# Optimization experiments

Measured on AMD Instinct MI355X. Metric: run time of the kernel, lower is better.

Reference implementation:

```python
import jax, jax.numpy as jnp
import numpy as np


def setup_inputs() -> dict:
    key = jax.random.key(0)
    ks = jax.random.split(key, 5)
    B, C, H, W = 4, 64, 64, 64
    C8 = C // 8
    return {
        "x_opt": jax.random.normal(ks[0], (B, C, H, W), jnp.float32),
        "x_sar": jax.random.normal(ks[1], (B, C, H, W), jnp.float32),
        "wq": jax.random.normal(ks[2], (C8, C), jnp.float32) * 0.05,
        "bq": jnp.zeros((C8,), jnp.float32),
        "wk": jax.random.normal(ks[3], (C8, C), jnp.float32) * 0.05,
        "bk": jnp.zeros((C8,), jnp.float32),
        "wv": jax.random.normal(ks[4], (C, C), jnp.float32) * 0.05,
        "bv": jnp.zeros((C,), jnp.float32),
        "gamma": jnp.zeros((1,), jnp.float32),
    }


def reference(x_opt, x_sar, wq, bq, wk, bk, wv, bv, gamma):
    b, c, h, w = x_opt.shape
    n = h * w
    xo = x_opt.reshape(b, c, n)  # [b, c, N]
    xs = x_sar.reshape(b, c, n)
    # 1x1 convs == channel matmuls
    q = jnp.einsum('oc,bcn->bon', wq, xo) + bq[None, :, None]  # [b, c//8, N]
    k = jnp.einsum('oc,bcn->bon', wk, xs) + bk[None, :, None]  # [b, c//8, N]
    v = jnp.einsum('oc,bcn->bon', wv, xs) + bv[None, :, None]  # [b, c, N]
    # attn[b, n, m] = softmax_m( q[:, :, n] . k[:, :, m] )  -- NO 1/sqrt(d) scaling
    scores = jnp.einsum('bdn,bdm->bnm', q, k)  # [b, N, N]
    attn = jax.nn.softmax(scores, axis=-1)
    # out[b, c, n] = sum_m v[b, c, m] * attn[b, n, m]
    out = jnp.einsum('bcm,bnm->bcn', v, attn).reshape(b, c, h, w)
    return gamma[0] * out + x_opt
```

## Files before the change

kernel.cpp:

```cpp
#include <hip/hip_runtime.h>
#include <hip/hip_bf16.h>
#include <stdint.h>

#define NDIM 4096
#define CDIM 64
#define NSPLIT 8
#define SPAN (NDIM / NSPLIT)
#define NQ4 (SPAN / 32)
#define LOG2E 1.44269504088896f

typedef float f32x4 __attribute__((ext_vector_type(4)));
typedef float f32x16 __attribute__((ext_vector_type(16)));
typedef short bf16x8 __attribute__((ext_vector_type(8)));
union U4B { uint4 u; bf16x8 b; };

static __device__ __forceinline__ uint32_t cvtpk(float lo, float hi) {
  uint32_t r;
  asm("v_cvt_pk_bf16_f32 %0, %1, %2" : "=v"(r) : "v"(lo), "v"(hi));
  return r;
}
static __device__ __forceinline__ uint16_t f2bf(float f) {
  uint32_t r;
  asm("v_cvt_pk_bf16_f32 %0, %1, %1" : "=v"(r) : "v"(f));
  return (uint16_t)r;
}
static __device__ __forceinline__ float fexp2(float x) {
  return __builtin_amdgcn_exp2f(x);
}

__global__ __launch_bounds__(256) void proj_kernel(
    const float* __restrict__ x_opt, const float* __restrict__ x_sar,
    const float* __restrict__ wq, const float* __restrict__ bq,
    const float* __restrict__ wk, const float* __restrict__ bk,
    const float* __restrict__ wvp, const float* __restrict__ bv,
    uint16_t* __restrict__ qf, uint16_t* __restrict__ kfp,
    uint16_t* __restrict__ vf2)
{
  const int tid = threadIdx.x;
  const int w = tid >> 6;
  const int l = tid & 63;
  const int x = l & 31;
  const int hi = l >> 5;

  const int id = blockIdx.x;
  const int b = id >> 7;
  const int n0 = (id & 127) * 32;
  const size_t xbase = (size_t)b * CDIM * NDIM;

  const float* xsrc = (w == 2) ? x_opt : x_sar;
  bf16x8 xB[4];
#pragma unroll
  for (int kc = 0; kc < 4; kc++) {
    float sv[8];
#pragma unroll
    for (int j = 0; j < 8; j++)
      sv[j] = xsrc[xbase + (size_t)(kc * 16 + hi * 8 + j) * NDIM + n0 + x];
    U4B us;
    us.u = make_uint4(cvtpk(sv[0], sv[1]), cvtpk(sv[2], sv[3]),
                      cvtpk(sv[4], sv[5]), cvtpk(sv[6], sv[7]));
    xB[kc] = us.b;
  }

  bf16x8 aF[4];
#pragma unroll
  for (int kc = 0; kc < 4; kc++) {
    U4B ua;
    ua.u = make_uint4(0u, 0u, 0u, 0u);
    if (w < 2) {
      const float* wr = wvp + (w * 32 + x) * 64 + kc * 16 + hi * 8;
      float4 wa = ((const float4*)wr)[0];
      float4 wb = ((const float4*)wr)[1];
      ua.u = make_uint4(cvtpk(wa.x, wa.y), cvtpk(wa.z, wa.w),
                        cvtpk(wb.x, wb.y), cvtpk(wb.z, wb.w));
    } else if (x < 8) {
      const float* wr = ((w == 2) ? wq : wk) + x * 64 + kc * 16 + hi * 8;
      float4 wa = ((const float4*)wr)[0];
      float4 wb = ((const float4*)wr)[1];
      ua.u = make_uint4(cvtpk(wa.x, wa.y), cvtpk(wa.z, wa.w),
                        cvtpk(wb.x, wb.y), cvtpk(wb.z, wb.w));
    }
    aF[kc] = ua.b;
  }

  const f32x16 z16 = {0.f,0.f,0.f,0.f, 0.f,0.f,0.f,0.f,
                      0.f,0.f,0.f,0.f, 0.f,0.f,0.f,0.f};
  f32x16 acc = z16;
#pragma unroll
  for (int kc = 0; kc < 4; kc++)
    acc = __builtin_amdgcn_mfma_f32_32x32x16_bf16(aF[kc], xB[kc], acc, 0, 0, 0);

  if (w < 2) {
    const size_t kbbase = (size_t)b * 256 + (n0 >> 4) + (x >> 4);
    const int kk = x & 15;
#pragma unroll
    for (int r = 0; r < 16; r++) {
      const int row = w * 32 + (r & 3) + 8 * (r >> 2) + 4 * hi;
      vf2[(kbbase * 64 + row) * 16 + kk] = f2bf(acc[r] + bv[row]);
    }
  } else if (w == 2) {
    float gv[4];
#pragma unroll
    for (int r = 0; r < 4; r++) gv[r] = (acc[r] + bq[4 * hi + r]) * LOG2E;
    const size_t nrow = ((size_t)b * NDIM + n0 + x) * 16;
    uint2 st;
    st.x = cvtpk(gv[0], gv[1]); st.y = cvtpk(gv[2], gv[3]);
    *(uint2*)(qf + nrow + hi * 4) = st;
    if (hi == 0) {
      const uint4 z4 = make_uint4(0u, 0u, 0u, 0u);
      *(uint4*)(qf + nrow + 8) = z4;
    }
  } else {
    float gv[4];
#pragma unroll
    for (int r = 0; r < 4; r++) gv[r] = acc[r] + bk[4 * hi + r];
    uint2 st;
    st.x = cvtpk(gv[0], gv[1]); st.y = cvtpk(gv[2], gv[3]);
    *(uint2*)(kfp + ((size_t)b * NDIM + n0 + x) * 8 + hi * 4) = st;
  }
}

__global__ __launch_bounds__(256, 4) void attn_kernel(
    const uint16_t* __restrict__ qf, const uint16_t* __restrict__ kfp,
    const uint16_t* __restrict__ vf2,
    uint16_t* __restrict__ po2, float* __restrict__ ls)
{
  const int tid = threadIdx.x;
  const int w = tid >> 6;
  const int l = tid & 63;
  const int x = l & 31;
  const int hi = l >> 5;

  const int id = blockIdx.x;
  const int x8 = id & 7;
  const int j  = id >> 3;
  const int b  = x8 & 3;
  const int sp = ((x8 >> 2) << 2) | ((j >> 2) & 3);
  const int qb = (j & 3) | (((j >> 4) & 7) << 2);

  const int n0 = qb * 128;
  const int qrow = n0 + w * 32 + x;

  U4B qfr;
  qfr.u = *(const uint4*)(qf + ((size_t)b * NDIM + qrow) * 16 + hi * 8);

  const uint16_t* ksb = kfp + ((size_t)b * NDIM + sp * SPAN) * 8;
  const uint16_t* vsb = vf2 + (((size_t)b * 256 + sp * 32) * 64) * 16;
  const int klane = x * 8;
  const int vlane = x * 16 + hi * 8;

  const f32x16 z16 = {0.f,0.f,0.f,0.f, 0.f,0.f,0.f,0.f,
                      0.f,0.f,0.f,0.f, 0.f,0.f,0.f,0.f};
  f32x16 oacc0 = z16, oacc1 = z16;
  float lacc[4] = {0.f, 0.f, 0.f, 0.f};

  uint4 kA  = *(const uint4*)(ksb + klane);
  uint4 vA0 = *(const uint4*)(vsb + vlane);
  uint4 vA1 = *(const uint4*)(vsb + 512 + vlane);
  uint4 vA2 = *(const uint4*)(vsb + 1024 + vlane);
  uint4 vA3 = *(const uint4*)(vsb + 1536 + vlane);

#pragma unroll
  for (int gq = 0; gq < NQ4; gq++) {
    const int e1 = (gq + 1) & 15;
    uint4 kn  = *(const uint4*)(ksb + e1 * 256 + klane);
    uint4 vn0 = *(const uint4*)(vsb + e1 * 2048 + vlane);
    uint4 vn1 = *(const uint4*)(vsb + e1 * 2048 + 512 + vlane);
    uint4 vn2 = *(const uint4*)(vsb + e1 * 2048 + 1024 + vlane);
    uint4 vn3 = *(const uint4*)(vsb + e1 * 2048 + 1536 + vlane);

    U4B ka; ka.u = kA;
    f32x16 s = __builtin_amdgcn_mfma_f32_32x32x16_bf16(ka.b, qfr.b, z16, 0, 0, 0);

    uint32_t W[8];
#pragma unroll
    for (int jj = 0; jj < 8; jj++) {
      const float p0 = fexp2(s[2 * jj]);
      const float p1 = fexp2(s[2 * jj + 1]);
      W[jj] = cvtpk(p0, p1);
      lacc[jj & 3] += p0 + p1;
    }

    __builtin_amdgcn_s_setprio(1);
    {
      uint32_t a0 = W[0], b0 = W[2], a1 = W[1], b1 = W[3];
      asm("v_permlane32_swap_b32 %0, %1" : "+v"(a0), "+v"(b0));
      asm("v_permlane32_swap_b32 %0, %1" : "+v"(a1), "+v"(b1));
      U4B pf, va, vb;
      pf.u = make_uint4(a0, a1, b0, b1);
      va.u = vA0; vb.u = vA1;
      oacc0 = __builtin_amdgcn_mfma_f32_32x32x16_bf16(va.b, pf.b, oacc0, 0, 0, 0);
      oacc1 = __builtin_amdgcn_mfma_f32_32x32x16_bf16(vb.b, pf.b, oacc1, 0, 0, 0);
    }
    {
      uint32_t a0 = W[4], b0 = W[6], a1 = W[5], b1 = W[7];
      asm("v_permlane32_swap_b32 %0, %1" : "+v"(a0), "+v"(b0));
      asm("v_permlane32_swap_b32 %0, %1" : "+v"(a1), "+v"(b1));
      U4B pf, va, vb;
      pf.u = make_uint4(a0, a1, b0, b1);
      va.u = vA2; vb.u = vA3;
      oacc0 = __builtin_amdgcn_mfma_f32_32x32x16_bf16(va.b, pf.b, oacc0, 0, 0, 0);
      oacc1 = __builtin_amdgcn_mfma_f32_32x32x16_bf16(vb.b, pf.b, oacc1, 0, 0, 0);
    }
    __builtin_amdgcn_s_setprio(0);

    kA = kn; vA0 = vn0; vA1 = vn1; vA2 = vn2; vA3 = vn3;
  }

  {
    uint16_t* pb = po2 + ((size_t)(sp * 256 + b * 64 + hi * 4)) * NDIM + qrow;
#pragma unroll
    for (int r = 0; r < 16; r++) {
      const size_t off = (size_t)((r & 3) + 8 * (r >> 2)) * NDIM;
      pb[off] = f2bf(oacc0[r]);
      pb[off + (size_t)32 * NDIM] = f2bf(oacc1[r]);
    }
  }
  float ltot = (lacc[0] + lacc[1]) + (lacc[2] + lacc[3]);
  ltot += __shfl_xor(ltot, 32);
  if (hi == 0)
    ls[((size_t)sp * 4 + b) * NDIM + qrow] = ltot;
}

__global__ __launch_bounds__(256) void merge_kernel(
    const uint16_t* __restrict__ po2, const float* __restrict__ ls,
    const float* __restrict__ x_opt, const float* __restrict__ gamma,
    float* __restrict__ out)
{
  const int idx = blockIdx.x * 256 + threadIdx.x;
  const int n8 = (idx & 511) << 3;
  const int row = idx >> 9;
  const int b = row >> 6;

  float acc[8] = {0.f, 0.f, 0.f, 0.f, 0.f, 0.f, 0.f, 0.f};
  f32x4 ws0 = {0.f, 0.f, 0.f, 0.f};
  f32x4 ws1 = {0.f, 0.f, 0.f, 0.f};
#pragma unroll
  for (int s = 0; s < NSPLIT; s++) {
    const uint4 pv = *(const uint4*)(po2 + ((size_t)s * 256 + row) * NDIM + n8);
    const uint32_t* pw = (const uint32_t*)&pv;
#pragma unroll
    for (int j = 0; j < 4; j++) {
      acc[j * 2 + 0] += __uint_as_float(pw[j] << 16);
      acc[j * 2 + 1] += __uint_as_float(pw[j] & 0xFFFF0000u);
    }
    const float* lp = ls + ((size_t)s * 4 + b) * NDIM + n8;
    ws0 += *(const f32x4*)(lp);
    ws1 += *(const f32x4*)(lp + 4);
  }
  const float gm = gamma[0];
  const float* xp = x_opt + (size_t)row * NDIM + n8;
  float* op = out + (size_t)row * NDIM + n8;
  float4 x0 = ((const float4*)xp)[0];
  float4 x1 = ((const float4*)xp)[1];
  float4 o0, o1;
  o0.x = gm * acc[0] / ws0[0] + x0.x;
  o0.y = gm * acc[1] / ws0[1] + x0.y;
  o0.z = gm * acc[2] / ws0[2] + x0.z;
  o0.w = gm * acc[3] / ws0[3] + x0.w;
  o1.x = gm * acc[4] / ws1[0] + x1.x;
  o1.y = gm * acc[5] / ws1[1] + x1.y;
  o1.z = gm * acc[6] / ws1[2] + x1.z;
  o1.w = gm * acc[7] / ws1[3] + x1.w;
  ((float4*)op)[0] = o0;
  ((float4*)op)[1] = o1;
}

extern "C" void kernel_launch(void* const* d_in, const int* in_sizes, int n_in,
                              void* d_out, int out_size, void* d_ws, size_t ws_size,
                              hipStream_t stream) {
  const float* x_opt = (const float*)d_in[0];
  const float* x_sar = (const float*)d_in[1];
  const float* wq    = (const float*)d_in[2];
  const float* bq    = (const float*)d_in[3];
  const float* wk    = (const float*)d_in[4];
  const float* bk    = (const float*)d_in[5];
  const float* wvp   = (const float*)d_in[6];
  const float* bv    = (const float*)d_in[7];
  const float* gamma = (const float*)d_in[8];
  float* outp = (float*)d_out;

  uint16_t* qf  = (uint16_t*)d_ws;
  uint16_t* kfp = (uint16_t*)((char*)d_ws + 524288);
  uint16_t* vf2 = (uint16_t*)((char*)d_ws + 1048576);
  uint16_t* po2 = (uint16_t*)((char*)d_ws + 3145728);
  float* lsp    = (float*)((char*)d_ws + 19922944);

  proj_kernel<<<512, 256, 0, stream>>>(x_opt, x_sar, wq, bq, wk, bk, wvp, bv,
                                       qf, kfp, vf2);
  attn_kernel<<<1024, 256, 0, stream>>>(qf, kfp, vf2, po2, lsp);
  merge_kernel<<<512, 256, 0, stream>>>(po2, lsp, x_opt, gamma, outp);
}
```

Measured before the change: 36.75 us.

## Process two query tiles per wave to reuse K/V fragments across queries

Each wave now handles 64 query rows as two 32-row MFMA fragments. Every K and V fragment loaded from global memory feeds both, which halves K/V load traffic per unit of work. The grid halves to 512 blocks, the block-to-(batch, split, query) mapping is simplified, and launch bounds drop to 2 blocks per CU to make room for the extra accumulators. In exchange, occupancy and latency hiding fall, and register pressure rises.

```diff
diff --git a/kernel.cpp b/kernel.cpp
--- a/kernel.cpp
+++ b/kernel.cpp
@@ -119,7 +119,7 @@
   }
 }
 
-__global__ __launch_bounds__(256, 4) void attn_kernel(
+__global__ __launch_bounds__(256, 2) void attn_kernel(
     const uint16_t* __restrict__ qf, const uint16_t* __restrict__ kfp,
     const uint16_t* __restrict__ vf2,
     uint16_t* __restrict__ po2, float* __restrict__ ls)
@@ -131,17 +131,16 @@
   const int hi = l >> 5;
 
   const int id = blockIdx.x;
-  const int x8 = id & 7;
-  const int j  = id >> 3;
-  const int b  = x8 & 3;
-  const int sp = ((x8 >> 2) << 2) | ((j >> 2) & 3);
-  const int qb = (j & 3) | (((j >> 4) & 7) << 2);
-
-  const int n0 = qb * 128;
-  const int qrow = n0 + w * 32 + x;
-
-  U4B qfr;
-  qfr.u = *(const uint4*)(qf + ((size_t)b * NDIM + qrow) * 16 + hi * 8);
+  const int sp = id & 7;
+  const int qb = (id >> 3) & 15;
+  const int b = id >> 7;
+
+  const int n0 = qb * 256;
+  const int qrow0 = n0 + w * 64 + x;
+
+  U4B qfr0, qfr1;
+  qfr0.u = *(const uint4*)(qf + ((size_t)b * NDIM + qrow0) * 16 + hi * 8);
+  qfr1.u = *(const uint4*)(qf + ((size_t)b * NDIM + qrow0 + 32) * 16 + hi * 8);
 
   const uint16_t* ksb = kfp + ((size_t)b * NDIM + sp * SPAN) * 8;
   const uint16_t* vsb = vf2 + (((size_t)b * 256 + sp * 32) * 64) * 16;
@@ -150,8 +149,10 @@
 
   const f32x16 z16 = {0.f,0.f,0.f,0.f, 0.f,0.f,0.f,0.f,
                       0.f,0.f,0.f,0.f, 0.f,0.f,0.f,0.f};
-  f32x16 oacc0 = z16, oacc1 = z16;
-  float lacc[4] = {0.f, 0.f, 0.f, 0.f};
+  f32x16 oacc00 = z16, oacc01 = z16;
+  f32x16 oacc10 = z16, oacc11 = z16;
+  float lacc0[4] = {0.f, 0.f, 0.f, 0.f};
+  float lacc1[4] = {0.f, 0.f, 0.f, 0.f};
 
   uint4 kA  = *(const uint4*)(ksb + klane);
   uint4 vA0 = *(const uint4*)(vsb + vlane);
@@ -168,57 +169,75 @@
     uint4 vn2 = *(const uint4*)(vsb + e1 * 2048 + 1024 + vlane);
     uint4 vn3 = *(const uint4*)(vsb + e1 * 2048 + 1536 + vlane);
 
-    U4B ka; ka.u = kA;
-    f32x16 s = __builtin_amdgcn_mfma_f32_32x32x16_bf16(ka.b, qfr.b, z16, 0, 0, 0);
-
-    uint32_t W[8];
-#pragma unroll
-    for (int jj = 0; jj < 8; jj++) {
-      const float p0 = fexp2(s[2 * jj]);
-      const float p1 = fexp2(s[2 * jj + 1]);
-      W[jj] = cvtpk(p0, p1);
-      lacc[jj & 3] += p0 + p1;
-    }
-
-    __builtin_amdgcn_s_setprio(1);
-    {
-      uint32_t a0 = W[0], b0 = W[2], a1 = W[1], b1 = W[3];
-      asm("v_permlane32_swap_b32 %0, %1" : "+v"(a0), "+v"(b0));
-      asm("v_permlane32_swap_b32 %0, %1" : "+v"(a1), "+v"(b1));
-      U4B pf, va, vb;
-      pf.u = make_uint4(a0, a1, b0, b1);
-      va.u = vA0; vb.u = vA1;
-      oacc0 = __builtin_amdgcn_mfma_f32_32x32x16_bf16(va.b, pf.b, oacc0, 0, 0, 0);
-      oacc1 = __builtin_amdgcn_mfma_f32_32x32x16_bf16(vb.b, pf.b, oacc1, 0, 0, 0);
-    }
-    {
-      uint32_t a0 = W[4], b0 = W[6], a1 = W[5], b1 = W[7];
-      asm("v_permlane32_swap_b32 %0, %1" : "+v"(a0), "+v"(b0));
-      asm("v_permlane32_swap_b32 %0, %1" : "+v"(a1), "+v"(b1));
-      U4B pf, va, vb;
-      pf.u = make_uint4(a0, a1, b0, b1);
-      va.u = vA2; vb.u = vA3;
-      oacc0 = __builtin_amdgcn_mfma_f32_32x32x16_bf16(va.b, pf.b, oacc0, 0, 0, 0);
-      oacc1 = __builtin_amdgcn_mfma_f32_32x32x16_bf16(vb.b, pf.b, oacc1, 0, 0, 0);
-    }
-    __builtin_amdgcn_s_setprio(0);
+#pragma unroll
+    for (int f = 0; f < 2; f++) {
+      U4B ka; ka.u = kA;
+      f32x16 s = __builtin_amdgcn_mfma_f32_32x32x16_bf16(
+          ka.b, (f == 0) ? qfr0.b : qfr1.b, z16, 0, 0, 0);
+
+      uint32_t W[8];
+#pragma unroll
+      for (int jj = 0; jj < 8; jj++) {
+        const float p0 = fexp2(s[2 * jj]);
+        const float p1 = fexp2(s[2 * jj + 1]);
+        W[jj] = cvtpk(p0, p1);
+        if (f == 0) lacc0[jj & 3] += p0 + p1;
+        else        lacc1[jj & 3] += p0 + p1;
+      }
+
+      __builtin_amdgcn_s_setprio(1);
+      {
+        uint32_t a0 = W[0], b0 = W[2], a1 = W[1], b1 = W[3];
+        asm("v_permlane32_swap_b32 %0, %1" : "+v"(a0), "+v"(b0));
+        asm("v_permlane32_swap_b32 %0, %1" : "+v"(a1), "+v"(b1));
+        U4B pf, va, vb;
+        pf.u = make_uint4(a0, a1, b0, b1);
+        va.u = vA0; vb.u = vA1;
+        if (f == 0) {
+          oacc00 = __builtin_amdgcn_mfma_f32_32x32x16_bf16(va.b, pf.b, oacc00, 0, 0, 0);
+          oacc01 = __builtin_amdgcn_mfma_f32_32x32x16_bf16(vb.b, pf.b, oacc01, 0, 0, 0);
+        } else {
+          oacc10 = __builtin_amdgcn_mfma_f32_32x32x16_bf16(va.b, pf.b, oacc10, 0, 0, 0);
+          oacc11 = __builtin_amdgcn_mfma_f32_32x32x16_bf16(vb.b, pf.b, oacc11, 0, 0, 0);
+        }
+      }
+      {
+        uint32_t a0 = W[4], b0 = W[6], a1 = W[5], b1 = W[7];
+        asm("v_permlane32_swap_b32 %0, %1" : "+v"(a0), "+v"(b0));
+        asm("v_permlane32_swap_b32 %0, %1" : "+v"(a1), "+v"(b1));
+        U4B pf, va, vb;
+        pf.u = make_uint4(a0, a1, b0, b1);
+        va.u = vA2; vb.u = vA3;
+        if (f == 0) {
+          oacc00 = __builtin_amdgcn_mfma_f32_32x32x16_bf16(va.b, pf.b, oacc00, 0, 0, 0);
+          oacc01 = __builtin_amdgcn_mfma_f32_32x32x16_bf16(vb.b, pf.b, oacc01, 0, 0, 0);
+        } else {
+          oacc10 = __builtin_amdgcn_mfma_f32_32x32x16_bf16(va.b, pf.b, oacc10, 0, 0, 0);
+          oacc11 = __builtin_amdgcn_mfma_f32_32x32x16_bf16(vb.b, pf.b, oacc11, 0, 0, 0);
+        }
+      }
+      __builtin_amdgcn_s_setprio(0);
+    }
 
     kA = kn; vA0 = vn0; vA1 = vn1; vA2 = vn2; vA3 = vn3;
   }
 
-  {
+#pragma unroll
+  for (int f = 0; f < 2; f++) {
+    const int qrow = qrow0 + f * 32;
     uint16_t* pb = po2 + ((size_t)(sp * 256 + b * 64 + hi * 4)) * NDIM + qrow;
 #pragma unroll
     for (int r = 0; r < 16; r++) {
       const size_t off = (size_t)((r & 3) + 8 * (r >> 2)) * NDIM;
-      pb[off] = f2bf(oacc0[r]);
-      pb[off + (size_t)32 * NDIM] = f2bf(oacc1[r]);
-    }
-  }
-  float ltot = (lacc[0] + lacc[1]) + (lacc[2] + lacc[3]);
-  ltot += __shfl_xor(ltot, 32);
-  if (hi == 0)
-    ls[((size_t)sp * 4 + b) * NDIM + qrow] = ltot;
+      pb[off] = f2bf(f == 0 ? oacc00[r] : oacc10[r]);
+      pb[off + (size_t)32 * NDIM] = f2bf(f == 0 ? oacc01[r] : oacc11[r]);
+    }
+    float ltot = (f == 0) ? (lacc0[0] + lacc0[1]) + (lacc0[2] + lacc0[3])
+                          : (lacc1[0] + lacc1[1]) + (lacc1[2] + lacc1[3]);
+    ltot += __shfl_xor(ltot, 32);
+    if (hi == 0)
+      ls[((size_t)sp * 4 + b) * NDIM + qrow] = ltot;
+  }
 }
 
 __global__ __launch_bounds__(256) void merge_kernel(
@@ -287,6 +306,6 @@
 
   proj_kernel<<<512, 256, 0, stream>>>(x_opt, x_sar, wq, bq, wk, bk, wvp, bv,
                                        qf, kfp, vf2);
-  attn_kernel<<<1024, 256, 0, stream>>>(qf, kfp, vf2, po2, lsp);
+  attn_kernel<<<512, 256, 0, stream>>>(qf, kfp, vf2, po2, lsp);
   merge_kernel<<<512, 256, 0, stream>>>(po2, lsp, x_opt, gamma, outp);
 }
```

New measurement: 51.26 us. +39.5%, slower.
